# Kernel tuning notes

Measured on AMD Instinct MI355X. Metric: run time of the kernel, lower is better.

The kernel has to match this reference:

```python
import jax, jax.numpy as jnp
import numpy as np

B, H, W, N, DX, DZ = 4, 64, 64, 4096, 2, 128
INIT_LS = 0.1


def setup_inputs() -> dict:
    key = jax.random.key(0)
    k1, k2, k3, k4 = jax.random.split(key, 4)
    xc_off_grid = jax.random.uniform(k1, (B, N, DX), dtype=jnp.float32)
    # regular grid coordinates in [0, 1]^2, broadcast over batch
    gy, gx = jnp.meshgrid(jnp.linspace(0.0, 1.0, H), jnp.linspace(0.0, 1.0, W), indexing="ij")
    xc_on_grid = jnp.broadcast_to(jnp.stack([gy, gx], axis=-1)[None], (B, H, W, DX)).astype(jnp.float32)
    zc_off_grid = jax.random.normal(k2, (B, N, DZ), dtype=jnp.float32)
    zc_on_grid = jax.random.normal(k3, (B, H, W, DZ), dtype=jnp.float32)
    # lengthscale_param = log(exp(init_lengthscale) - 1)  (inverse softplus)
    lengthscale_param = jnp.log(jnp.expm1(jnp.full((DX,), INIT_LS, dtype=jnp.float32)))
    return {
        "xc_off_grid": xc_off_grid,
        "xc_on_grid": xc_on_grid,
        "zc_off_grid": zc_off_grid,
        "zc_on_grid": zc_on_grid,
        "lengthscale_param": lengthscale_param,
        "ignore_on_grid": 0,
    }


def reference(xc_off_grid, xc_on_grid, zc_off_grid, zc_on_grid, lengthscale_param, ignore_on_grid):
    b = xc_on_grid.shape[0]
    grid_shape = xc_on_grid.shape[1:-1]
    dz = zc_off_grid.shape[-1]
    xg = xc_on_grid.reshape(b, -1, xc_on_grid.shape[-1])  # [b, m, dx]
    lengthscale = 1e-05 + jax.nn.softplus(lengthscale_param)  # [dx]
    # squared scaled distances: [b, m, n]
    diff = (xg[:, :, None, :] - xc_off_grid[:, None, :, :]) / lengthscale
    weights = jnp.exp(-0.5 * jnp.sum(diff * diff, axis=-1))  # [b, m, n]
    zc = jnp.einsum("bmn,bnd->bmd", weights, zc_off_grid)  # [b, m, dz]
    if not ignore_on_grid:
        zc = zc + zc_on_grid.reshape(b, -1, dz)
    return zc.reshape((b,) + grid_shape + (dz,))
```

## Files before the change

### kernel.cpp

```cpp
#include <hip/hip_runtime.h>

#define HH 64
#define WW 64
#define NN 4096
#define DZc 128
#define KS 8
#define BK 64
#define NKT (NN / KS / BK)
#define CELLS 2097152
#define ZT_BYTES (4ull * 128 * 4096 * 2ull)
#define WS_NEED (ZT_BYTES + 8ull * CELLS * 2ull)

typedef __fp16 v2fp16 __attribute__((ext_vector_type(2)));
typedef _Float16 v4h __attribute__((ext_vector_type(4)));
typedef _Float16 v8h __attribute__((ext_vector_type(8)));
typedef float v16f __attribute__((ext_vector_type(16)));
typedef double v2d __attribute__((ext_vector_type(2)));

__device__ __forceinline__ unsigned pk16(float lo, float hi){
  union { v2fp16 h; unsigned u; } c;
  c.h = __builtin_amdgcn_cvt_pkrtz(lo, hi);
  return c.u;
}
__device__ __forceinline__ float fexp2(float x){ return __builtin_amdgcn_exp2f(x); }

__global__ __launch_bounds__(256, 8)
void init_out_kernel(const float4* __restrict__ zc_on,
                     const int* __restrict__ ignore,
                     float4* __restrict__ out){
  int i = blockIdx.x * blockDim.x + threadIdx.x;
  float4 v = zc_on[i];
  if (ignore[0]) { v.x = 0.f; v.y = 0.f; v.z = 0.f; v.w = 0.f; }
  out[i] = v;
}

__global__ __launch_bounds__(256, 4)
void prepack_kernel(const float* __restrict__ zc_off, _Float16* __restrict__ zt_g){
  __shared__ unsigned tt[128 * 34];
  const int bidx = blockIdx.x;
  const int b  = bidx >> 6;
  const int n0 = (bidx & 63) * 64;
  const int t  = threadIdx.x;

  const int np = t >> 3;
  const int d0 = (t & 7) * 16;
  const float* r0 = zc_off + ((size_t)(b * NN + n0 + 2 * np)) * DZc + d0;
  float4 a[4], c[4];
  #pragma unroll
  for (int i = 0; i < 4; ++i){
    a[i] = *(const float4*)&r0[4 * i];
    c[i] = *(const float4*)&r0[DZc + 4 * i];
  }
  const float* af = (const float*)a;
  const float* cf = (const float*)c;
  #pragma unroll
  for (int j = 0; j < 16; ++j)
    tt[(d0 + j) * 34 + np] = pk16(af[j], cf[j]);

  __syncthreads();

  const int d  = t >> 1;
  const int nh = t & 1;
  const unsigned* rr = tt + d * 34 + nh * 16;
  _Float16* w = zt_g + ((size_t)(b * DZc + d)) * NN + n0 + nh * 32;
  double v[8];
  #pragma unroll
  for (int j = 0; j < 8; ++j) v[j] = *(const double*)&rr[2 * j];
  #pragma unroll
  for (int j = 0; j < 4; ++j){
    v2d s; s[0] = v[2 * j]; s[1] = v[2 * j + 1];
    *(v2d*)&w[8 * j] = s;
  }
}

__global__ __launch_bounds__(256, 8)
void reduce_kernel(const v8h* __restrict__ part,
                   const float4* __restrict__ zc_on,
                   const int* __restrict__ ignore,
                   float4* __restrict__ out){
  int i = blockIdx.x * blockDim.x + threadIdx.x;
  float4 s0 = zc_on[2 * i];
  float4 s1 = zc_on[2 * i + 1];
  if (ignore[0]) {
    s0.x = s0.y = s0.z = s0.w = 0.f;
    s1.x = s1.y = s1.z = s1.w = 0.f;
  }
  #pragma unroll
  for (int ks = 0; ks < KS; ++ks){
    v8h p = part[(size_t)ks * (CELLS / 8) + i];
    s0.x += (float)p[0]; s0.y += (float)p[1]; s0.z += (float)p[2]; s0.w += (float)p[3];
    s1.x += (float)p[4]; s1.y += (float)p[5]; s1.z += (float)p[6]; s1.w += (float)p[7];
  }
  out[2 * i]     = s0;
  out[2 * i + 1] = s1;
}

template<bool PRE>
__global__ __launch_bounds__(512, 4)
void setconv_gemm_kernel(const float* __restrict__ xc_off,
                         const float* __restrict__ xc_on,
                         const float* __restrict__ zc_off,
                         const _Float16* __restrict__ zpack,
                         const float* __restrict__ lsp,
                         _Float16* __restrict__ part,
                         float* __restrict__ out)
{
  __shared__ unsigned short zt[2][128][68];
  __shared__ unsigned short gt[2][40][72];

  const int tid = threadIdx.x;
  const int bid = blockIdx.x;
  const int ks  = bid >> 6;
  const int bm  = bid & 63;
  const int b   = bm >> 4;
  const int mt  = bm & 15;
  const int iy0 = (mt >> 3) * 32;
  const int ix0 = (mt & 7) * 8;
  const int nbase = ks * (NN / KS);

  const float lsy = 1e-5f + log1pf(expf(lsp[0]));
  const float lsx = 1e-5f + log1pf(expf(lsp[1]));
  const float LOG2E = 1.44269504088896340736f;
  const float ay = -0.5f * LOG2E / (lsy * lsy);
  const float ax = -0.5f * LOG2E / (lsx * lsx);

  const int gp = tid & 31;
  const int gr = tid >> 5;
  float gc[3], ga[3];
  #pragma unroll
  for (int i = 0; i < 3; ++i){
    int row = gr + 16 * i;
    if (row < 32)      { gc[i] = xc_on[((b * HH + iy0 + row) * WW) * 2];        ga[i] = ay; }
    else if (row < 40) { gc[i] = xc_on[(b * HH * WW + ix0 + row - 32) * 2 + 1]; ga[i] = ax; }
    else               { gc[i] = 0.f; ga[i] = 0.f; }
  }

  const int zd = tid & 127;
  const int zq = tid >> 7;
  const _Float16* ztg = PRE ? (zpack + ((size_t)(b * DZc + zd)) * NN + nbase + zq * 16)
                            : (const _Float16*)nullptr;

  const int lane = tid & 63;
  const int wv  = tid >> 6;
  const int mq  = wv >> 1;
  const int dh  = wv & 1;
  const int l31 = lane & 31;
  const int lh  = lane >> 5;
  const int gxr = 32 + (l31 & 7);
  const int gyr = mq * 8 + (l31 >> 3);
  const int dbase = dh * 64;

  v16f acc[2][2];
  #pragma unroll
  for (int m = 0; m < 2; ++m)
    #pragma unroll
    for (int d = 0; d < 2; ++d)
      #pragma unroll
      for (int r = 0; r < 16; ++r)
        acc[m][d][r] = 0.f;

  const float* xb = xc_off + (size_t)b * NN * 2;
  const float* zb = zc_off + (size_t)b * NN * DZc;

  {
    const int n0 = nbase;
    float4 xq = *(const float4*)&xb[(size_t)(n0 + 2 * gp) * 2];
    unsigned* gw = (unsigned*)&gt[0][0][0];
    #pragma unroll
    for (int i = 0; i < 3; ++i){
      int row = gr + 16 * i;
      if (row < 40){
        float s0 = (row < 32) ? xq.x : xq.y;
        float s1 = (row < 32) ? xq.z : xq.w;
        float d0 = gc[i] - s0, d1 = gc[i] - s1;
        gw[row * 36 + gp] = pk16(fexp2(ga[i] * d0 * d0), fexp2(ga[i] * d1 * d1));
      }
    }
    if (PRE){
      #pragma unroll
      for (int i = 0; i < 2; ++i){
        union { v8h v; double d[2]; } u;
        u.v = *(const v8h*)&ztg[8 * i];
        *(double*)&zt[0][zd][zq * 16 + 8 * i]     = u.d[0];
        *(double*)&zt[0][zd][zq * 16 + 8 * i + 4] = u.d[1];
      }
    } else {
      float zv[16];
      #pragma unroll
      for (int i = 0; i < 16; ++i)
        zv[i] = zb[(size_t)(n0 + zq * 16 + i) * DZc + zd];
      #pragma unroll
      for (int j = 0; j < 4; ++j){
        union { unsigned u[2]; double d; } w;
        w.u[0] = pk16(zv[4 * j],     zv[4 * j + 1]);
        w.u[1] = pk16(zv[4 * j + 2], zv[4 * j + 3]);
        *(double*)&zt[0][zd][zq * 16 + 4 * j] = w.d;
      }
    }
  }
  __syncthreads();

  #pragma unroll 1
  for (int kt = 0; kt < NKT; ++kt){
    const int buf  = kt & 1;
    const int nbuf = buf ^ 1;
    const bool have_next = (kt + 1 < NKT);
    const int n1 = nbase + (kt + 1) * BK;

    v8h zrn[2];
    float zv[16];
    float4 xq_n = (float4){0.f, 0.f, 0.f, 0.f};
    if (have_next){
      if (PRE){
        #pragma unroll
        for (int i = 0; i < 2; ++i)
          zrn[i] = *(const v8h*)&ztg[(kt + 1) * BK + 8 * i];
      } else {
        #pragma unroll
        for (int i = 0; i < 16; ++i)
          zv[i] = zb[(size_t)(n1 + zq * 16 + i) * DZc + zd];
      }
      xq_n = *(const float4*)&xb[(size_t)(n1 + 2 * gp) * 2];
    }

    __builtin_amdgcn_s_setprio(1);
    #pragma unroll
    for (int kstep = 0; kstep < 4; ++kstep){
      const int k0 = kstep * 16 + lh * 8;
      const v8h xu = *(const v8h*)&gt[buf][gxr][k0];
      v8h bfr[2];
      #pragma unroll
      for (int dtl = 0; dtl < 2; ++dtl){
        union { v4h h[2]; v8h v; } zu;
        zu.h[0] = *(const v4h*)&zt[buf][dbase + dtl * 32 + l31][k0];
        zu.h[1] = *(const v4h*)&zt[buf][dbase + dtl * 32 + l31][k0 + 4];
        bfr[dtl] = zu.v;
      }
      #pragma unroll
      for (int mtl = 0; mtl < 2; ++mtl){
        const v8h yu = *(const v8h*)&gt[buf][gyr + mtl * 4][k0];
        v8h av = yu * xu;
        #pragma unroll
        for (int dtl = 0; dtl < 2; ++dtl)
          acc[mtl][dtl] = __builtin_amdgcn_mfma_f32_32x32x16_f16(av, bfr[dtl], acc[mtl][dtl], 0, 0, 0);
      }
    }
    __builtin_amdgcn_s_setprio(0);

    if (have_next){
      if (PRE){
        #pragma unroll
        for (int i = 0; i < 2; ++i){
          union { v8h v; double d[2]; } u;
          u.v = zrn[i];
          *(double*)&zt[nbuf][zd][zq * 16 + 8 * i]     = u.d[0];
          *(double*)&zt[nbuf][zd][zq * 16 + 8 * i + 4] = u.d[1];
        }
      } else {
        #pragma unroll
        for (int j = 0; j < 4; ++j){
          union { unsigned u[2]; double d; } w;
          w.u[0] = pk16(zv[4 * j],     zv[4 * j + 1]);
          w.u[1] = pk16(zv[4 * j + 2], zv[4 * j + 3]);
          *(double*)&zt[nbuf][zd][zq * 16 + 4 * j] = w.d;
        }
      }
      unsigned* gw = (unsigned*)&gt[nbuf][0][0];
      #pragma unroll
      for (int i = 0; i < 3; ++i){
        int row = gr + 16 * i;
        if (row < 40){
          float s0 = (row < 32) ? xq_n.x : xq_n.y;
          float s1 = (row < 32) ? xq_n.z : xq_n.w;
          float d0 = gc[i] - s0, d1 = gc[i] - s1;
          gw[row * 36 + gp] = pk16(fexp2(ga[i] * d0 * d0), fexp2(ga[i] * d1 * d1));
        }
      }
    }
    __syncthreads();
  }

  if (part){
    _Float16* pw = part + (size_t)ks * CELLS;
    #pragma unroll
    for (int mtl = 0; mtl < 2; ++mtl)
      #pragma unroll
      for (int dtl = 0; dtl < 2; ++dtl){
        const int d = dbase + dtl * 32 + l31;
        #pragma unroll
        for (int reg = 0; reg < 16; ++reg){
          const int row = (reg & 3) + 8 * (reg >> 2) + 4 * lh;
          const int m = mq * 64 + mtl * 32 + row;
          const int iy = iy0 + (m >> 3);
          const int ix = ix0 + (m & 7);
          pw[((b * HH + iy) * WW + ix) * DZc + d] = (_Float16)acc[mtl][dtl][reg];
        }
      }
  } else {
    #pragma unroll
    for (int mtl = 0; mtl < 2; ++mtl)
      #pragma unroll
      for (int dtl = 0; dtl < 2; ++dtl){
        const int d = dbase + dtl * 32 + l31;
        #pragma unroll
        for (int reg = 0; reg < 16; ++reg){
          const int row = (reg & 3) + 8 * (reg >> 2) + 4 * lh;
          const int m = mq * 64 + mtl * 32 + row;
          const int iy = iy0 + (m >> 3);
          const int ix = ix0 + (m & 7);
          unsafeAtomicAdd(&out[((b * HH + iy) * WW + ix) * DZc + d], acc[mtl][dtl][reg]);
        }
      }
  }
}

extern "C" void kernel_launch(void* const* d_in, const int* in_sizes, int n_in,
                              void* d_out, int out_size, void* d_ws, size_t ws_size,
                              hipStream_t stream){
  const float* xc_off = (const float*)d_in[0];
  const float* xc_on  = (const float*)d_in[1];
  const float* zc_off = (const float*)d_in[2];
  const float* zc_on  = (const float*)d_in[3];
  const float* lsp    = (const float*)d_in[4];
  const int*   ign    = (const int*)d_in[5];
  float* out = (float*)d_out;

  if (ws_size >= WS_NEED){
    _Float16* zpack = (_Float16*)d_ws;
    _Float16* part  = (_Float16*)((char*)d_ws + ZT_BYTES);
    prepack_kernel<<<4 * 64, 256, 0, stream>>>(zc_off, zpack);
    setconv_gemm_kernel<true><<<KS * 64, 512, 0, stream>>>(xc_off, xc_on, zc_off, zpack, lsp, part, out);
    reduce_kernel<<<CELLS / 8 / 256, 256, 0, stream>>>((const v8h*)part, (const float4*)zc_on, ign, (float4*)out);
  } else {
    init_out_kernel<<<CELLS / 4 / 256, 256, 0, stream>>>((const float4*)zc_on, ign, (float4*)out);
    setconv_gemm_kernel<false><<<KS * 64, 512, 0, stream>>>(xc_off, xc_on, zc_off, nullptr, lsp, nullptr, out);
  }
}
```

Measured before the change: 105.2 us.

## Prepack zc into MFMA fragment layout and read B operands directly from global

Measured after the change: 107.0 us. About the same (+1.6%).

```diff
diff --git a/kernel.cpp b/kernel.cpp
--- a/kernel.cpp
+++ b/kernel.cpp
@@ -15,7 +15,6 @@
 typedef _Float16 v4h __attribute__((ext_vector_type(4)));
 typedef _Float16 v8h __attribute__((ext_vector_type(8)));
 typedef float v16f __attribute__((ext_vector_type(16)));
-typedef double v2d __attribute__((ext_vector_type(2)));
 
 __device__ __forceinline__ unsigned pk16(float lo, float hi){
   union { v2fp16 h; unsigned u; } c;
@@ -35,11 +34,12 @@
 }
 
 __global__ __launch_bounds__(256, 4)
-void prepack_kernel(const float* __restrict__ zc_off, _Float16* __restrict__ zt_g){
-  __shared__ unsigned tt[128 * 34];
+void prepack_kernel(const float* __restrict__ zc_off, _Float16* __restrict__ zf){
+  __shared__ unsigned tt[128 * 36];
   const int bidx = blockIdx.x;
   const int b  = bidx >> 6;
-  const int n0 = (bidx & 63) * 64;
+  const int nt = bidx & 63;
+  const int n0 = nt * 64;
   const int t  = threadIdx.x;
 
   const int np = t >> 3;
@@ -55,21 +55,19 @@
   const float* cf = (const float*)c;
   #pragma unroll
   for (int j = 0; j < 16; ++j)
-    tt[(d0 + j) * 34 + np] = pk16(af[j], cf[j]);
+    tt[(d0 + j) * 36 + np] = pk16(af[j], cf[j]);
 
   __syncthreads();
 
-  const int d  = t >> 1;
-  const int nh = t & 1;
-  const unsigned* rr = tt + d * 34 + nh * 16;
-  _Float16* w = zt_g + ((size_t)(b * DZc + d)) * NN + n0 + nh * 32;
-  double v[8];
-  #pragma unroll
-  for (int j = 0; j < 8; ++j) v[j] = *(const double*)&rr[2 * j];
-  #pragma unroll
-  for (int j = 0; j < 4; ++j){
-    v2d s; s[0] = v[2 * j]; s[1] = v[2 * j + 1];
-    *(v2d*)&w[8 * j] = s;
+  const int dblk = t >> 6;
+  const int q    = t & 63;
+  const int d    = dblk * 32 + (q >> 1);
+  const int lh   = q & 1;
+  _Float16* ob = zf + ((size_t)(b * 64 + nt)) * 8192;
+  #pragma unroll
+  for (int p = 0; p < 4; ++p){
+    uint4 w = *(const uint4*)&tt[d * 36 + p * 8 + lh * 4];
+    *(uint4*)&ob[(size_t)((p * 4 + dblk) * 64 + q) * 8] = w;
   }
 }
 
@@ -95,15 +93,145 @@
   out[2 * i + 1] = s1;
 }
 
-template<bool PRE>
+__global__ __launch_bounds__(256, 4)
+void setconv_gemm_pre(const float* __restrict__ xc_off,
+                      const float* __restrict__ xc_on,
+                      const _Float16* __restrict__ zpack,
+                      const float* __restrict__ lsp,
+                      _Float16* __restrict__ part)
+{
+  __shared__ unsigned short gt[2][24][72];
+
+  const int tid = threadIdx.x;
+  const int rawb = blockIdx.x;
+  const int lb = (rawb & 7) * 128 + (rawb >> 3);
+  const int ks = lb >> 7;
+  const int bm = lb & 127;
+  const int b  = bm >> 5;
+  const int mt = bm & 31;
+  const int iy0 = (mt >> 3) * 16;
+  const int ix0 = (mt & 7) * 8;
+
+  const float lsy = 1e-5f + log1pf(expf(lsp[0]));
+  const float lsx = 1e-5f + log1pf(expf(lsp[1]));
+  const float LOG2E = 1.44269504088896340736f;
+  const float ay = -0.5f * LOG2E / (lsy * lsy);
+  const float ax = -0.5f * LOG2E / (lsx * lsx);
+
+  const int gp = tid & 31;
+  const int gr = tid >> 5;
+  float gc[3], ga[3];
+  #pragma unroll
+  for (int i = 0; i < 3; ++i){
+    int row = gr + 8 * i;
+    if (row < 16){ gc[i] = xc_on[((b * HH + iy0 + row) * WW) * 2];        ga[i] = ay; }
+    else         { gc[i] = xc_on[(b * HH * WW + ix0 + row - 16) * 2 + 1]; ga[i] = ax; }
+  }
+
+  const int lane = tid & 63;
+  const int wv  = tid >> 6;
+  const int mq  = wv >> 1;
+  const int dh  = wv & 1;
+  const int l31 = lane & 31;
+  const int lh  = lane >> 5;
+  const int gxr = 16 + (l31 & 7);
+  const int gyr = mq * 8 + (l31 >> 3);
+  const int dblk0 = dh * 2;
+  const int q = l31 * 2 + lh;
+
+  v16f acc[2][2];
+  #pragma unroll
+  for (int m = 0; m < 2; ++m)
+    #pragma unroll
+    for (int d = 0; d < 2; ++d)
+      #pragma unroll
+      for (int r = 0; r < 16; ++r)
+        acc[m][d][r] = 0.f;
+
+  const float* xb = xc_off + (size_t)b * NN * 2;
+  const _Float16* zb0 = zpack + ((size_t)(b * 64 + ks * NKT)) * 8192
+                              + (size_t)(dblk0 * 64 + q) * 8;
+
+  {
+    float4 xq = *(const float4*)&xb[(size_t)(ks * (NN / KS) + 2 * gp) * 2];
+    unsigned* gw = (unsigned*)&gt[0][0][0];
+    #pragma unroll
+    for (int i = 0; i < 3; ++i){
+      int row = gr + 8 * i;
+      float s0 = (row < 16) ? xq.x : xq.y;
+      float s1 = (row < 16) ? xq.z : xq.w;
+      float d0 = gc[i] - s0, d1 = gc[i] - s1;
+      gw[row * 36 + gp] = pk16(fexp2(ga[i] * d0 * d0), fexp2(ga[i] * d1 * d1));
+    }
+  }
+  __syncthreads();
+
+  #pragma unroll 1
+  for (int kt = 0; kt < NKT; ++kt){
+    const int buf  = kt & 1;
+    const int nbuf = buf ^ 1;
+    const bool have_next = (kt + 1 < NKT);
+
+    float4 xq_n = (float4){0.f, 0.f, 0.f, 0.f};
+    if (have_next)
+      xq_n = *(const float4*)&xb[(size_t)(ks * (NN / KS) + (kt + 1) * BK + 2 * gp) * 2];
+
+    const _Float16* zk = zb0 + (size_t)kt * 8192;
+
+    __builtin_amdgcn_s_setprio(1);
+    #pragma unroll
+    for (int kstep = 0; kstep < 4; ++kstep){
+      const int k0 = kstep * 16 + lh * 8;
+      const v8h xu = *(const v8h*)&gt[buf][gxr][k0];
+      const v8h bf0 = *(const v8h*)&zk[kstep * 2048];
+      const v8h bf1 = *(const v8h*)&zk[kstep * 2048 + 512];
+      #pragma unroll
+      for (int mtl = 0; mtl < 2; ++mtl){
+        const v8h yu = *(const v8h*)&gt[buf][gyr + mtl * 4][k0];
+        v8h av = yu * xu;
+        acc[mtl][0] = __builtin_amdgcn_mfma_f32_32x32x16_f16(av, bf0, acc[mtl][0], 0, 0, 0);
+        acc[mtl][1] = __builtin_amdgcn_mfma_f32_32x32x16_f16(av, bf1, acc[mtl][1], 0, 0, 0);
+      }
+    }
+    __builtin_amdgcn_s_setprio(0);
+
+    if (have_next){
+      unsigned* gw = (unsigned*)&gt[nbuf][0][0];
+      #pragma unroll
+      for (int i = 0; i < 3; ++i){
+        int row = gr + 8 * i;
+        float s0 = (row < 16) ? xq_n.x : xq_n.y;
+        float s1 = (row < 16) ? xq_n.z : xq_n.w;
+        float d0 = gc[i] - s0, d1 = gc[i] - s1;
+        gw[row * 36 + gp] = pk16(fexp2(ga[i] * d0 * d0), fexp2(ga[i] * d1 * d1));
+      }
+    }
+    __syncthreads();
+  }
+
+  _Float16* pw = part + (size_t)ks * CELLS;
+  #pragma unroll
+  for (int mtl = 0; mtl < 2; ++mtl)
+    #pragma unroll
+    for (int dtl = 0; dtl < 2; ++dtl){
+      const int d = dh * 64 + dtl * 32 + l31;
+      #pragma unroll
+      for (int reg = 0; reg < 16; ++reg){
+        const int row = (reg & 3) + 8 * (reg >> 2) + 4 * lh;
+        const int m = mq * 64 + mtl * 32 + row;
+        const int iy = iy0 + (m >> 3);
+        const int ix = ix0 + (m & 7);
+        pw[((b * HH + iy) * WW + ix) * DZc + d] = (_Float16)acc[mtl][dtl][reg];
+      }
+    }
+}
+
 __global__ __launch_bounds__(512, 4)
-void setconv_gemm_kernel(const float* __restrict__ xc_off,
-                         const float* __restrict__ xc_on,
-                         const float* __restrict__ zc_off,
-                         const _Float16* __restrict__ zpack,
-                         const float* __restrict__ lsp,
-                         _Float16* __restrict__ part,
-                         float* __restrict__ out)
+void setconv_gemm_fb(const float* __restrict__ xc_off,
+                     const float* __restrict__ xc_on,
+                     const float* __restrict__ zc_off,
+                     const float* __restrict__ lsp,
+                     float* __restrict__ out)
 {
   __shared__ unsigned short zt[2][128][68];
   __shared__ unsigned short gt[2][40][72];
@@ -137,8 +265,6 @@
 
   const int zd = tid & 127;
   const int zq = tid >> 7;
-  const _Float16* ztg = PRE ? (zpack + ((size_t)(b * DZc + zd)) * NN + nbase + zq * 16)
-                            : (const _Float16*)nullptr;
 
   const int lane = tid & 63;
   const int wv  = tid >> 6;
@@ -176,26 +302,16 @@
         gw[row * 36 + gp] = pk16(fexp2(ga[i] * d0 * d0), fexp2(ga[i] * d1 * d1));
       }
     }
-    if (PRE){
-      #pragma unroll
-      for (int i = 0; i < 2; ++i){
-        union { v8h v; double d[2]; } u;
-        u.v = *(const v8h*)&ztg[8 * i];
-        *(double*)&zt[0][zd][zq * 16 + 8 * i]     = u.d[0];
-        *(double*)&zt[0][zd][zq * 16 + 8 * i + 4] = u.d[1];
-      }
-    } else {
-      float zv[16];
-      #pragma unroll
-      for (int i = 0; i < 16; ++i)
-        zv[i] = zb[(size_t)(n0 + zq * 16 + i) * DZc + zd];
-      #pragma unroll
-      for (int j = 0; j < 4; ++j){
-        union { unsigned u[2]; double d; } w;
-        w.u[0] = pk16(zv[4 * j],     zv[4 * j + 1]);
-        w.u[1] = pk16(zv[4 * j + 2], zv[4 * j + 3]);
-        *(double*)&zt[0][zd][zq * 16 + 4 * j] = w.d;
-      }
+    float zv[16];
+    #pragma unroll
+    for (int i = 0; i < 16; ++i)
+      zv[i] = zb[(size_t)(n0 + zq * 16 + i) * DZc + zd];
+    #pragma unroll
+    for (int j = 0; j < 4; ++j){
+      union { unsigned u[2]; double dd; } w;
+      w.u[0] = pk16(zv[4 * j],     zv[4 * j + 1]);
+      w.u[1] = pk16(zv[4 * j + 2], zv[4 * j + 3]);
+      *(double*)&zt[0][zd][zq * 16 + 4 * j] = w.dd;
     }
   }
   __syncthreads();
@@ -207,23 +323,15 @@
     const bool have_next = (kt + 1 < NKT);
     const int n1 = nbase + (kt + 1) * BK;
 
-    v8h zrn[2];
     float zv[16];
     float4 xq_n = (float4){0.f, 0.f, 0.f, 0.f};
     if (have_next){
-      if (PRE){
-        #pragma unroll
-        for (int i = 0; i < 2; ++i)
-          zrn[i] = *(const v8h*)&ztg[(kt + 1) * BK + 8 * i];
-      } else {
-        #pragma unroll
-        for (int i = 0; i < 16; ++i)
-          zv[i] = zb[(size_t)(n1 + zq * 16 + i) * DZc + zd];
-      }
+      #pragma unroll
+      for (int i = 0; i < 16; ++i)
+        zv[i] = zb[(size_t)(n1 + zq * 16 + i) * DZc + zd];
       xq_n = *(const float4*)&xb[(size_t)(n1 + 2 * gp) * 2];
     }
 
-    __builtin_amdgcn_s_setprio(1);
     #pragma unroll
     for (int kstep = 0; kstep < 4; ++kstep){
       const int k0 = kstep * 16 + lh * 8;
@@ -245,25 +353,14 @@
           acc[mtl][dtl] = __builtin_amdgcn_mfma_f32_32x32x16_f16(av, bfr[dtl], acc[mtl][dtl], 0, 0, 0);
       }
     }
-    __builtin_amdgcn_s_setprio(0);
 
     if (have_next){
-      if (PRE){
-        #pragma unroll
-        for (int i = 0; i < 2; ++i){
-          union { v8h v; double d[2]; } u;
-          u.v = zrn[i];
-          *(double*)&zt[nbuf][zd][zq * 16 + 8 * i]     = u.d[0];
-          *(double*)&zt[nbuf][zd][zq * 16 + 8 * i + 4] = u.d[1];
-        }
-      } else {
-        #pragma unroll
-        for (int j = 0; j < 4; ++j){
-          union { unsigned u[2]; double d; } w;
-          w.u[0] = pk16(zv[4 * j],     zv[4 * j + 1]);
-          w.u[1] = pk16(zv[4 * j + 2], zv[4 * j + 3]);
-          *(double*)&zt[nbuf][zd][zq * 16 + 4 * j] = w.d;
-        }
+      #pragma unroll
+      for (int j = 0; j < 4; ++j){
+        union { unsigned u[2]; double dd; } w;
+        w.u[0] = pk16(zv[4 * j],     zv[4 * j + 1]);
+        w.u[1] = pk16(zv[4 * j + 2], zv[4 * j + 3]);
+        *(double*)&zt[nbuf][zd][zq * 16 + 4 * j] = w.dd;
       }
       unsigned* gw = (unsigned*)&gt[nbuf][0][0];
       #pragma unroll
@@ -280,38 +377,20 @@
     __syncthreads();
   }
 
-  if (part){
-    _Float16* pw = part + (size_t)ks * CELLS;
-    #pragma unroll
-    for (int mtl = 0; mtl < 2; ++mtl)
-      #pragma unroll
-      for (int dtl = 0; dtl < 2; ++dtl){
-        const int d = dbase + dtl * 32 + l31;
-        #pragma unroll
-        for (int reg = 0; reg < 16; ++reg){
-          const int row = (reg & 3) + 8 * (reg >> 2) + 4 * lh;
-          const int m = mq * 64 + mtl * 32 + row;
-          const int iy = iy0 + (m >> 3);
-          const int ix = ix0 + (m & 7);
-          pw[((b * HH + iy) * WW + ix) * DZc + d] = (_Float16)acc[mtl][dtl][reg];
-        }
-      }
-  } else {
-    #pragma unroll
-    for (int mtl = 0; mtl < 2; ++mtl)
-      #pragma unroll
-      for (int dtl = 0; dtl < 2; ++dtl){
-        const int d = dbase + dtl * 32 + l31;
-        #pragma unroll
-        for (int reg = 0; reg < 16; ++reg){
-          const int row = (reg & 3) + 8 * (reg >> 2) + 4 * lh;
-          const int m = mq * 64 + mtl * 32 + row;
-          const int iy = iy0 + (m >> 3);
-          const int ix = ix0 + (m & 7);
-          unsafeAtomicAdd(&out[((b * HH + iy) * WW + ix) * DZc + d], acc[mtl][dtl][reg]);
-        }
-      }
-  }
+  #pragma unroll
+  for (int mtl = 0; mtl < 2; ++mtl)
+    #pragma unroll
+    for (int dtl = 0; dtl < 2; ++dtl){
+      const int d = dbase + dtl * 32 + l31;
+      #pragma unroll
+      for (int reg = 0; reg < 16; ++reg){
+        const int row = (reg & 3) + 8 * (reg >> 2) + 4 * lh;
+        const int m = mq * 64 + mtl * 32 + row;
+        const int iy = iy0 + (m >> 3);
+        const int ix = ix0 + (m & 7);
+        unsafeAtomicAdd(&out[((b * HH + iy) * WW + ix) * DZc + d], acc[mtl][dtl][reg]);
+      }
+    }
 }
 
 extern "C" void kernel_launch(void* const* d_in, const int* in_sizes, int n_in,
@@ -329,10 +408,10 @@
     _Float16* zpack = (_Float16*)d_ws;
     _Float16* part  = (_Float16*)((char*)d_ws + ZT_BYTES);
     prepack_kernel<<<4 * 64, 256, 0, stream>>>(zc_off, zpack);
-    setconv_gemm_kernel<true><<<KS * 64, 512, 0, stream>>>(xc_off, xc_on, zc_off, zpack, lsp, part, out);
+    setconv_gemm_pre<<<KS * 128, 256, 0, stream>>>(xc_off, xc_on, zpack, lsp, part);
     reduce_kernel<<<CELLS / 8 / 256, 256, 0, stream>>>((const v8h*)part, (const float4*)zc_on, ign, (float4*)out);
   } else {
     init_out_kernel<<<CELLS / 4 / 256, 256, 0, stream>>>((const float4*)zc_on, ign, (float4*)out);
-    setconv_gemm_kernel<false><<<KS * 64, 512, 0, stream>>>(xc_off, xc_on, zc_off, nullptr, lsp, nullptr, out);
-  }
-}
+    setconv_gemm_fb<<<KS * 64, 512, 0, stream>>>(xc_off, xc_on, zc_off, lsp, out);
+  }
+}
```
